# Kernel optimization log

Hardware: AMD Instinct MI355X
Metric: run time of the kernel (lower is better)

## Reference

```python
import jax, jax.numpy as jnp
import numpy as np

B, T, J, D = 64, 2048, 128, 256

def setup_inputs() -> dict:
    key = jax.random.key(0)
    k1, k2, k3 = jax.random.split(key, 3)
    H = jax.random.normal(k1, (B, T, D), dtype=jnp.float32)
    U = jax.random.normal(k2, (B, J, D), dtype=jnp.float32)
    w = jax.random.normal(k3, (3 * D, 1), dtype=jnp.float32) * 0.05
    return {"H": H, "U": U, "w": w}


def reference(H, U, w):
    # Original: tile H to (B,T,J,D), tile U to (B,T,J,D), concat [H,U,H*U] -> (B,T,J,3D),
    # then dot with w (3D,1) and squeeze -> (B,T,J).
    # Equivalent trilinear form without materializing the tiled tensor:
    # S[b,t,j] = H[b,t]@w1 + U[b,j]@w2 + (H[b,t]*w3)@U[b,j]
    d = H.shape[-1]
    wv = w[:, 0]
    w1, w2, w3 = wv[:d], wv[d:2 * d], wv[2 * d:]
    s_h = jnp.einsum('btd,d->bt', H, w1)          # (B,T)
    s_u = jnp.einsum('bjd,d->bj', U, w2)          # (B,J)
    s_hu = jnp.einsum('btd,bjd->btj', H * w3, U)  # (B,T,J)
    return s_h[:, :, None] + s_u[:, None, :] + s_hu
```

## Files before the change

### kernel.cpp

```cpp
#include <hip/hip_runtime.h>
#include <stdint.h>

#define Bb 64
#define Tt 2048
#define Jj 128
#define Dd 256


typedef __attribute__((ext_vector_type(8))) __bf16 bf16x8;
typedef __attribute__((ext_vector_type(8))) unsigned short ushort8v;
typedef __attribute__((ext_vector_type(4))) float f32x4;

__device__ __forceinline__ unsigned short f2bf(float f) {
    unsigned int u = __builtin_bit_cast(unsigned int, f);
    u += 0x7FFFu + ((u >> 16) & 1u);
    return (unsigned short)(u >> 16);
}

__device__ __forceinline__ bf16x8 pack8(const float4& a0, const float4& a1) {
    bf16x8 r;
    r[0] = (__bf16)a0.x; r[1] = (__bf16)a0.y; r[2] = (__bf16)a0.z; r[3] = (__bf16)a0.w;
    r[4] = (__bf16)a1.x; r[5] = (__bf16)a1.y; r[6] = (__bf16)a1.z; r[7] = (__bf16)a1.w;
    return r;
}

__global__ __launch_bounds__(512)
__attribute__((amdgpu_waves_per_eu(4, 4)))
void sim_fused(const float* __restrict__ H, const float* __restrict__ U,
               const float* __restrict__ w, float* __restrict__ out) {
    __shared__ ushort8v lUp[4608];
    __shared__ float    lsu[Jj];

    const int tid   = threadIdx.x;
    const int wid   = tid >> 6;
    const int lane  = tid & 63;
    const int row16 = lane & 15;
    const int quad  = lane >> 4;

    const int o     = blockIdx.x;
    const int b     = (o & 7) * 8 + ((o >> 3) & 7);
    const int mbase = (o >> 6) * 256;

    const float* Hbase = H + ((size_t)(b * Tt + mbase + wid * 16 + row16)) * Dd + quad * 8;
    float4 hb0[8], hb1[8];
#pragma unroll
    for (int p = 0; p < 8; ++p) {
        hb0[p] = *(const float4*)(Hbase + p * 32);
        hb1[p] = *(const float4*)(Hbase + p * 32 + 4);
    }

    const float* Urow = U + ((size_t)(b * Jj + wid * 16 + row16)) * Dd + quad * 8;
    float sup = 0.f;
#pragma unroll
    for (int p = 0; p < 8; ++p) {
        const float4 u0 = *(const float4*)(Urow + p * 32);
        const float4 u1 = *(const float4*)(Urow + p * 32 + 4);
        const float* w3p = w + 2 * Dd + p * 32 + quad * 8;
        const float4 w30 = *(const float4*)(w3p);
        const float4 w31 = *(const float4*)(w3p + 4);
        const float* w2p = w + Dd + p * 32 + quad * 8;
        const float4 w20 = *(const float4*)(w2p);
        const float4 w21 = *(const float4*)(w2p + 4);
        ushort8v s;
        s[0] = f2bf(u0.x * w30.x); s[1] = f2bf(u0.y * w30.y);
        s[2] = f2bf(u0.z * w30.z); s[3] = f2bf(u0.w * w30.w);
        s[4] = f2bf(u1.x * w31.x); s[5] = f2bf(u1.y * w31.y);
        s[6] = f2bf(u1.z * w31.z); s[7] = f2bf(u1.w * w31.w);
        lUp[(wid * 8 + p) * 64 + lane] = s;
        sup += u0.x * w20.x + u0.y * w20.y + u0.z * w20.z + u0.w * w20.w
             + u1.x * w21.x + u1.y * w21.y + u1.z * w21.z + u1.w * w21.w;
    }
    {
        const int k0 = wid * 32 + quad * 8;
        const float4 w1a = *(const float4*)(w + k0);
        const float4 w1b = *(const float4*)(w + k0 + 4);
        const bool n0 = row16 == 0;
        ushort8v s;
        s[0] = n0 ? f2bf(w1a.x) : (unsigned short)0;
        s[1] = n0 ? f2bf(w1a.y) : (unsigned short)0;
        s[2] = n0 ? f2bf(w1a.z) : (unsigned short)0;
        s[3] = n0 ? f2bf(w1a.w) : (unsigned short)0;
        s[4] = n0 ? f2bf(w1b.x) : (unsigned short)0;
        s[5] = n0 ? f2bf(w1b.y) : (unsigned short)0;
        s[6] = n0 ? f2bf(w1b.z) : (unsigned short)0;
        s[7] = n0 ? f2bf(w1b.w) : (unsigned short)0;
        lUp[(8 * 8 + wid) * 64 + lane] = s;
    }
    sup += __shfl_xor(sup, 16);
    sup += __shfl_xor(sup, 32);
    if (lane < 16) lsu[wid * 16 + lane] = sup;

    f32x4 acc[9];
#pragma unroll
    for (int j = 0; j < 9; ++j) acc[j] = (f32x4){0.f, 0.f, 0.f, 0.f};

    __syncthreads();

#pragma unroll
    for (int mt = 0; mt < 2; ++mt) {
#pragma unroll
        for (int ks = 0; ks < 8; ++ks) {
            const float4 h0 = hb0[ks];
            const float4 h1 = hb1[ks];
            if (mt == 0) {
                const float* np = Hbase + (size_t)(128 * Dd) + ks * 32;
                hb0[ks] = *(const float4*)(np);
                hb1[ks] = *(const float4*)(np + 4);
            }

            const bf16x8 af = pack8(h0, h1);
#pragma unroll
            for (int j = 0; j < 9; ++j) {
                const bf16x8 bf = __builtin_bit_cast(bf16x8, lUp[(j * 8 + ks) * 64 + lane]);
                acc[j] = __builtin_amdgcn_mfma_f32_16x16x32_bf16(af, bf, acc[j], 0, 0, 0);
            }
        }

        float shv[4];
#pragma unroll
        for (int rg = 0; rg < 4; ++rg)
            shv[rg] = __shfl(acc[8][rg], quad * 16);

        float* outW = out + ((size_t)(b * Tt + mbase + mt * 128 + wid * 16)) * Jj;
#pragma unroll
        for (int j = 0; j < 8; ++j) {
            const int col = j * 16 + row16;
            const float suv = lsu[col];
#pragma unroll
            for (int rg = 0; rg < 4; ++rg)
                outW[(size_t)(quad * 4 + rg) * Jj + col] = acc[j][rg] + shv[rg] + suv;
        }

        if (mt == 0) {
#pragma unroll
            for (int j = 0; j < 9; ++j) acc[j] = (f32x4){0.f, 0.f, 0.f, 0.f};
        }
    }
}

extern "C" void kernel_launch(void* const* d_in, const int* in_sizes, int n_in,
                              void* d_out, int out_size, void* d_ws, size_t ws_size,
                              hipStream_t stream) {
    const float* H = (const float*)d_in[0];
    const float* U = (const float*)d_in[1];
    const float* w = (const float*)d_in[2];
    float* out = (float*)d_out;
    (void)d_ws; (void)ws_size;

    sim_fused<<<Bb * 8, 512, 0, stream>>>(H, U, w, out);
}
```

Before: 256.3 us.

## Split J across two blocks, shrink H prefetch, compute H·w1 on VALU

Each block now handles half of the J columns, which doubles the grid to 1024 blocks. U staging is split across waves along the K dimension, and the partial U·w2 sums are combined from two LDS slots. The H·w1 term moves out of the extra MFMA column tile into a VALU dot product with a shuffle reduction. H prefetch shrinks from 16 to 4 float4 registers per thread, and the fixed waves-per-EU attribute is dropped, both to cut register pressure and raise occupancy. The trade-off is that each H tile is read twice from global memory, and it adds redundant U preprocessing.

New measurement: 249.0 us. -2.8%, faster.

```diff
diff --git a/kernel.cpp b/kernel.cpp
--- a/kernel.cpp
+++ b/kernel.cpp
@@ -25,11 +25,10 @@
 }
 
 __global__ __launch_bounds__(512)
-__attribute__((amdgpu_waves_per_eu(4, 4)))
 void sim_fused(const float* __restrict__ H, const float* __restrict__ U,
                const float* __restrict__ w, float* __restrict__ out) {
-    __shared__ ushort8v lUp[4608];
-    __shared__ float    lsu[Jj];
+    __shared__ ushort8v lUp[2048];
+    __shared__ float    lsuP[128];
 
     const int tid   = threadIdx.x;
     const int wid   = tid >> 6;
@@ -39,26 +38,30 @@
 
     const int o     = blockIdx.x;
     const int b     = (o & 7) * 8 + ((o >> 3) & 7);
-    const int mbase = (o >> 6) * 256;
+    const int jh    = (o >> 6) & 1;
+    const int mbase = (o >> 7) * 256;
 
     const float* Hbase = H + ((size_t)(b * Tt + mbase + wid * 16 + row16)) * Dd + quad * 8;
-    float4 hb0[8], hb1[8];
+    float4 hb0[2], hb1[2];
 #pragma unroll
-    for (int p = 0; p < 8; ++p) {
+    for (int p = 0; p < 2; ++p) {
         hb0[p] = *(const float4*)(Hbase + p * 32);
         hb1[p] = *(const float4*)(Hbase + p * 32 + 4);
     }
 
-    const float* Urow = U + ((size_t)(b * Jj + wid * 16 + row16)) * Dd + quad * 8;
+    const int uj = wid & 3;
+    const int kh = wid >> 2;
+    const float* Urow = U + ((size_t)(b * Jj + jh * 64 + uj * 16 + row16)) * Dd
+                        + kh * 128 + quad * 8;
     float sup = 0.f;
 #pragma unroll
-    for (int p = 0; p < 8; ++p) {
+    for (int p = 0; p < 4; ++p) {
         const float4 u0 = *(const float4*)(Urow + p * 32);
         const float4 u1 = *(const float4*)(Urow + p * 32 + 4);
-        const float* w3p = w + 2 * Dd + p * 32 + quad * 8;
+        const float* w3p = w + 2 * Dd + kh * 128 + p * 32 + quad * 8;
         const float4 w30 = *(const float4*)(w3p);
         const float4 w31 = *(const float4*)(w3p + 4);
-        const float* w2p = w + Dd + p * 32 + quad * 8;
+        const float* w2p = w + Dd + kh * 128 + p * 32 + quad * 8;
         const float4 w20 = *(const float4*)(w2p);
         const float4 w21 = *(const float4*)(w2p + 4);
         ushort8v s;
@@ -66,66 +69,63 @@
         s[2] = f2bf(u0.z * w30.z); s[3] = f2bf(u0.w * w30.w);
         s[4] = f2bf(u1.x * w31.x); s[5] = f2bf(u1.y * w31.y);
         s[6] = f2bf(u1.z * w31.z); s[7] = f2bf(u1.w * w31.w);
-        lUp[(wid * 8 + p) * 64 + lane] = s;
+        lUp[(uj * 8 + kh * 4 + p) * 64 + lane] = s;
         sup += u0.x * w20.x + u0.y * w20.y + u0.z * w20.z + u0.w * w20.w
              + u1.x * w21.x + u1.y * w21.y + u1.z * w21.z + u1.w * w21.w;
     }
-    {
-        const int k0 = wid * 32 + quad * 8;
-        const float4 w1a = *(const float4*)(w + k0);
-        const float4 w1b = *(const float4*)(w + k0 + 4);
-        const bool n0 = row16 == 0;
-        ushort8v s;
-        s[0] = n0 ? f2bf(w1a.x) : (unsigned short)0;
-        s[1] = n0 ? f2bf(w1a.y) : (unsigned short)0;
-        s[2] = n0 ? f2bf(w1a.z) : (unsigned short)0;
-        s[3] = n0 ? f2bf(w1a.w) : (unsigned short)0;
-        s[4] = n0 ? f2bf(w1b.x) : (unsigned short)0;
-        s[5] = n0 ? f2bf(w1b.y) : (unsigned short)0;
-        s[6] = n0 ? f2bf(w1b.z) : (unsigned short)0;
-        s[7] = n0 ? f2bf(w1b.w) : (unsigned short)0;
-        lUp[(8 * 8 + wid) * 64 + lane] = s;
-    }
     sup += __shfl_xor(sup, 16);
     sup += __shfl_xor(sup, 32);
-    if (lane < 16) lsu[wid * 16 + lane] = sup;
+    if (lane < 16) lsuP[kh * 64 + uj * 16 + lane] = sup;
 
-    f32x4 acc[9];
+    f32x4 acc[4];
 #pragma unroll
-    for (int j = 0; j < 9; ++j) acc[j] = (f32x4){0.f, 0.f, 0.f, 0.f};
+    for (int j = 0; j < 4; ++j) acc[j] = (f32x4){0.f, 0.f, 0.f, 0.f};
 
     __syncthreads();
 
 #pragma unroll
     for (int mt = 0; mt < 2; ++mt) {
+        float sh = 0.f;
 #pragma unroll
         for (int ks = 0; ks < 8; ++ks) {
-            const float4 h0 = hb0[ks];
-            const float4 h1 = hb1[ks];
-            if (mt == 0) {
-                const float* np = Hbase + (size_t)(128 * Dd) + ks * 32;
-                hb0[ks] = *(const float4*)(np);
-                hb1[ks] = *(const float4*)(np + 4);
+            const int kk   = mt * 8 + ks;
+            const int slot = kk & 1;
+            const float4 h0 = hb0[slot];
+            const float4 h1 = hb1[slot];
+            if (kk < 14) {
+                const float* np = Hbase + (size_t)(((kk + 2) >> 3) * 128 * Dd)
+                                        + ((kk + 2) & 7) * 32;
+                hb0[slot] = *(const float4*)(np);
+                hb1[slot] = *(const float4*)(np + 4);
             }
+
+            const float* w1p = w + ks * 32 + quad * 8;
+            const float4 wa = *(const float4*)(w1p);
+            const float4 wb = *(const float4*)(w1p + 4);
+            sh += h0.x * wa.x + h0.y * wa.y + h0.z * wa.z + h0.w * wa.w
+                + h1.x * wb.x + h1.y * wb.y + h1.z * wb.z + h1.w * wb.w;
 
             const bf16x8 af = pack8(h0, h1);
 #pragma unroll
-            for (int j = 0; j < 9; ++j) {
+            for (int j = 0; j < 4; ++j) {
                 const bf16x8 bf = __builtin_bit_cast(bf16x8, lUp[(j * 8 + ks) * 64 + lane]);
                 acc[j] = __builtin_amdgcn_mfma_f32_16x16x32_bf16(af, bf, acc[j], 0, 0, 0);
             }
         }
 
+        float sh2 = sh;
+        sh2 += __shfl_xor(sh2, 16);
+        sh2 += __shfl_xor(sh2, 32);
         float shv[4];
 #pragma unroll
         for (int rg = 0; rg < 4; ++rg)
-            shv[rg] = __shfl(acc[8][rg], quad * 16);
+            shv[rg] = __shfl(sh2, quad * 4 + rg);
 
-        float* outW = out + ((size_t)(b * Tt + mbase + mt * 128 + wid * 16)) * Jj;
+        float* outW = out + ((size_t)(b * Tt + mbase + mt * 128 + wid * 16)) * Jj + jh * 64;
 #pragma unroll
-        for (int j = 0; j < 8; ++j) {
+        for (int j = 0; j < 4; ++j) {
             const int col = j * 16 + row16;
-            const float suv = lsu[col];
+            const float suv = lsuP[col] + lsuP[64 + col];
 #pragma unroll
             for (int rg = 0; rg < 4; ++rg)
                 outW[(size_t)(quad * 4 + rg) * Jj + col] = acc[j][rg] + shv[rg] + suv;
@@ -133,7 +133,7 @@
 
         if (mt == 0) {
 #pragma unroll
-            for (int j = 0; j < 9; ++j) acc[j] = (f32x4){0.f, 0.f, 0.f, 0.f};
+            for (int j = 0; j < 4; ++j) acc[j] = (f32x4){0.f, 0.f, 0.f, 0.f};
         }
     }
 }
@@ -147,5 +147,5 @@
     float* out = (float*)d_out;
     (void)d_ws; (void)ws_size;
 
-    sim_fused<<<Bb * 8, 512, 0, stream>>>(H, U, w, out);
+    sim_fused<<<Bb * 16, 512, 0, stream>>>(H, U, w, out);
 }
```
